# Optimization experiments

Hardware: AMD Instinct MI355X
Metric: run time of the kernel (lower is better)

Reference implementation:

```python
import jax, jax.numpy as jnp
import numpy as np

B, N, F, DM, DMO, OM, L = 32, 64, 64, 128, 64, 128, 4
PRE_H, PRE_O, POST_H = 128, 64, 64
E = N * N
EPS = 1e-5


def swish(x):
    return x * jax.nn.sigmoid(x)


def bn_edges(x, g, b):
    # BatchNorm1d(num_features=E) applied to [B, E, D]: per-edge-channel stats over (batch, D)
    m = x.mean(axis=(0, 2), keepdims=True)
    v = x.var(axis=(0, 2), keepdims=True)
    return (x - m) / jnp.sqrt(v + EPS) * g[None, :, None] + b[None, :, None]


def setup_inputs():
    key = jax.random.key(0)
    ks = iter(jax.random.split(key, 64))

    def rn(shape, s=0.05):
        return jax.random.normal(next(ks), shape, dtype=jnp.float32) * s

    # fully-connected graph incl. self-loops (required by BatchNorm1d(n_nodes^2))
    src, dst = np.meshgrid(np.arange(N), np.arange(N), indexing='ij')
    edge_index = jnp.asarray(np.stack([src.reshape(-1), dst.reshape(-1)]), dtype=jnp.int32)
    return {
        'node_feature': rn((B, N, F), 1.0),
        'vectors': rn((B, N, OM), 1.0),
        'edge_index': edge_index,
        'msg_W1': rn((L, 2 * F, DM)), 'msg_b1': rn((L, DM)),
        'bn1_g': jnp.ones((L, E), jnp.float32), 'bn1_b': jnp.zeros((L, E), jnp.float32),
        'msg_W2': rn((L, DM, DM)), 'msg_b2': rn((L, DM)),
        'bn2_g': jnp.ones((L, E), jnp.float32), 'bn2_b': jnp.zeros((L, E), jnp.float32),
        'msg_W3': rn((L, DM, DM)), 'msg_b3': rn((L, DM)),
        'bn3_g': jnp.ones((L, E), jnp.float32), 'bn3_b': jnp.zeros((L, E), jnp.float32),
        'msg_W4': rn((L, DM, DMO)), 'msg_b4': rn((L, DMO)),
        'upd_W1': rn((L, OM + F + DMO, DM)), 'upd_b1': rn((L, DM)),
        'upd_W2': rn((L, DM, DM)), 'upd_b2': rn((L, DM)),
        'upd_W3': rn((L, DM, DM)), 'upd_b3': rn((L, DM)),
        'upd_W4': rn((L, DM, F)), 'upd_b4': rn((L, F)),
        'pre_W1': rn((F, PRE_H)), 'pre_b1': rn((PRE_H,)),
        'pre_W2': rn((PRE_H, PRE_H)), 'pre_b2': rn((PRE_H,)),
        'pre_W3': rn((PRE_H, PRE_H)), 'pre_b3': rn((PRE_H,)),
        'pre_W4': rn((PRE_H, PRE_O)), 'pre_b4': rn((PRE_O,)),
        'post_W1': rn((PRE_O, POST_H)), 'post_b1': rn((POST_H,)),
        'post_W2': rn((POST_H, 1)), 'post_b2': rn((1,)),
    }


def reference(node_feature, vectors, edge_index,
              msg_W1, msg_b1, bn1_g, bn1_b, msg_W2, msg_b2, bn2_g, bn2_b,
              msg_W3, msg_b3, bn3_g, bn3_b, msg_W4, msg_b4,
              upd_W1, upd_b1, upd_W2, upd_b2, upd_W3, upd_b3, upd_W4, upd_b4,
              pre_W1, pre_b1, pre_W2, pre_b2, pre_W3, pre_b3, pre_W4, pre_b4,
              post_W1, post_b1, post_W2, post_b2):
    src, dst = edge_index[0], edge_index[1]
    x = node_feature  # [B, N, F]
    v = vectors       # [B, N, OM]
    cnt = jax.ops.segment_sum(jnp.ones((E,), jnp.float32), dst, num_segments=N)
    inv_cnt = 1.0 / jnp.maximum(cnt, 1.0)
    for l in range(L):
        x_i = x[:, dst]  # [B, E, F] gather targets
        x_j = x[:, src]  # [B, E, F] gather sources
        h = swish(jnp.concatenate([x_i, x_j], -1) @ msg_W1[l] + msg_b1[l])
        h = bn_edges(h, bn1_g[l], bn1_b[l])
        h = bn_edges(swish(h @ msg_W2[l] + msg_b2[l]), bn2_g[l], bn2_b[l])
        h = bn_edges(swish(h @ msg_W3[l] + msg_b3[l]), bn3_g[l], bn3_b[l])
        m = swish(h @ msg_W4[l] + msg_b4[l])  # [B, E, DMO]
        agg = jax.ops.segment_sum(jnp.transpose(m, (1, 0, 2)), dst, num_segments=N)
        agg = jnp.transpose(agg, (1, 0, 2)) * inv_cnt[None, :, None]  # mean aggr, [B, N, DMO]
        u = jnp.concatenate([v, x, agg], -1)  # [B, N, OM+F+DMO]
        h = swish(u @ upd_W1[l] + upd_b1[l])
        h = swish(h @ upd_W2[l] + upd_b2[l])
        h = swish(h @ upd_W3[l] + upd_b3[l])
        x = x + swish(h @ upd_W4[l] + upd_b4[l])  # residual update
    h = swish(x @ pre_W1 + pre_b1)
    h = swish(h @ pre_W2 + pre_b2)
    h = swish(h @ pre_W3 + pre_b3)
    h = h @ pre_W4 + pre_b4
    c = swish(h @ post_W1 + post_b1) @ post_W2 + post_b2  # [B, N, 1]
    x3 = jnp.einsum('bnd,bn->bd', v, c[..., 0])           # coefficient-weighted vector sum
    return x3, v, c
```

## Files before the change

kernel.cpp:

```cpp
#include <hip/hip_runtime.h>
#include <hip/hip_bf16.h>

typedef unsigned short u16t;
typedef __attribute__((ext_vector_type(8))) short bf16x8;
typedef __attribute__((ext_vector_type(4))) short bf16x4;
typedef __attribute__((ext_vector_type(4))) float f32x4;

#define Bn 32
#define Nn 64
#define Fd 64
#define DMd 128
#define DMOd 64
#define OMd 128
#define En 4096

#define NTEN 36
#define TOTALC 1073217
#define HP 136
#define UP 264
#define XP 72
#define WSEG 131072

__device__ const int kOffs[NTEN + 1] = {
    0,        131072,   393216,   458752,   459264,   475648,   492032,   557568,
    558080,   574464,   590848,   656384,   656896,   673280,   689664,   722432,
    722688,   853760,   854272,   919808,   920320,   985856,   986368,   1019136,
    1019392,  1027584,  1027712,  1044096,  1044224,  1060608,  1060736,  1068928,
    1068992,  1073088,  1073152,  1073216,  1073217
};

#define C_NF    0
#define C_VEC   131072
#define C_MW1   393216
#define C_MB1   458752
#define C_G1    459264
#define C_BB1   475648
#define C_MW2   492032
#define C_MB2   557568
#define C_G2    558080
#define C_BB2   574464
#define C_MW3   590848
#define C_MB3   656384
#define C_G3    656896
#define C_BB3   673280
#define C_MW4   689664
#define C_MB4   722432
#define C_UW1   722688
#define C_UB1   853760
#define C_UW2   854272
#define C_UB2   919808
#define C_UW3   920320
#define C_UB3   985856
#define C_UW4   986368
#define C_UB4   1019136
#define C_PW1   1019392
#define C_PB1   1027584
#define C_PW2   1027712
#define C_PB2   1044096
#define C_PW3   1044224
#define C_PB3   1060608
#define C_PW4   1060736
#define C_PB4   1068928
#define C_QW1   1068992
#define C_QB1   1073088
#define C_QW2   1073152
#define C_QB2   1073216

#define S_W2T 0
#define S_W3T 16384
#define S_W4T 32768
#define S_U1T 40960
#define S_U2T 73728
#define S_U3T 90112
#define S_U4T 106496
#define S_W1T 114688

struct Ptrs { const void* p[NTEN]; };

__device__ __forceinline__ float us2f(u16t u) {
    return __uint_as_float(((unsigned int)u) << 16);
}
__device__ __forceinline__ u16t f2us(float f) {
    __hip_bfloat16 h = __float2bfloat16(f);
    return *reinterpret_cast<u16t*>(&h);
}
__device__ __forceinline__ float swishf(float x) {
    return x * __builtin_amdgcn_rcpf(1.0f + __expf(-x));
}

__global__ void k_flag(const u16t* __restrict__ g1raw, int* __restrict__ flag) {
    if (threadIdx.x == 0) *flag = (g1raw[0] == 0x3F80u) ? 1 : 0;
}

__global__ __launch_bounds__(256) void k_convert(Ptrs t, float* __restrict__ C,
                                                 float* __restrict__ x,
                                                 const int* __restrict__ flagp) {
    int i = blockIdx.x * 256 + threadIdx.x;
    if (i >= TOTALC) return;
    const int flag = *flagp;
    int lo = 0, hi = NTEN;
    while (hi - lo > 1) { int m = (lo + hi) >> 1; if (i >= kOffs[m]) lo = m; else hi = m; }
    const int local = i - kOffs[lo];
    float v;
    if (flag) v = us2f(((const u16t*)t.p[lo])[local]);
    else      v = ((const float*)t.p[lo])[local];
    C[i] = v;
    if (i < Bn * Nn * Fd) x[i] = v;
}

__global__ __launch_bounds__(256) void k_prepw(const float* __restrict__ C,
                                               u16t* __restrict__ W) {
    int i = blockIdx.x * 256 + threadIdx.x;
    if (i >= 4 * WSEG) return;
    const int l = i / WSEG;
    int r = i - l * WSEG;
    int src;
    if (r < S_W3T)      { int q = r;          int n = q >> 7, k = q & 127; src = C_MW2 + l*16384 + k*128 + n; }
    else if (r < S_W4T) { int q = r - S_W3T;  int n = q >> 7, k = q & 127; src = C_MW3 + l*16384 + k*128 + n; }
    else if (r < S_U1T) { int q = r - S_W4T;  int n = q >> 7, k = q & 127; src = C_MW4 + l*8192  + k*64  + n; }
    else if (r < S_U2T) { int q = r - S_U1T;  int n = q >> 8, k = q & 255; src = C_UW1 + l*32768 + k*128 + n; }
    else if (r < S_U3T) { int q = r - S_U2T;  int n = q >> 7, k = q & 127; src = C_UW2 + l*16384 + k*128 + n; }
    else if (r < S_U4T) { int q = r - S_U3T;  int n = q >> 7, k = q & 127; src = C_UW3 + l*16384 + k*128 + n; }
    else if (r < S_W1T) { int q = r - S_U4T;  int n = q >> 7, k = q & 127; src = C_UW4 + l*8192  + k*64  + n; }
    else                { int q = r - S_W1T;  int n = q >> 7, k = q & 127; src = C_MW1 + l*16384 + k*128 + n; }
    W[i] = f2us(C[src]);
}

__global__ __launch_bounds__(256) void k_cs(const u16t* __restrict__ Wt,
                                            float* __restrict__ CS) {
    const int i = blockIdx.x * 256 + threadIdx.x;
    if (i >= 4 * 320) return;
    const int l = i / 320, j = i - l * 320;
    const u16t* base = Wt + l * WSEG +
        (j < 128 ? S_W2T + j * 128
                 : (j < 256 ? S_W3T + (j - 128) * 128
                            : S_W4T + (j - 256) * 128));
    float s = 0.f;
    #pragma unroll 8
    for (int k = 0; k < 128; k++) s += us2f(base[k]);
    CS[i] = s;
}

__global__ __launch_bounds__(128) void k_pq0(const float* __restrict__ x,
                                             const float* __restrict__ W1,
                                             float* __restrict__ P, float* __restrict__ Q,
                                             float* __restrict__ agg) {
    const int gid = blockIdx.x * 128 + threadIdx.x;
    if (gid < Bn * Nn * DMOd) agg[gid] = 0.f;
    __shared__ float xr[Fd];
    const int bn = blockIdx.x;
    const int tid = threadIdx.x;
    if (tid < Fd) xr[tid] = x[bn * Fd + tid];
    __syncthreads();
    float accP = 0.f, accQ = 0.f;
    #pragma unroll
    for (int k = 0; k < Fd; k++) {
        float xv = xr[k];
        accP += xv * W1[k * DMd + tid];
        accQ += xv * W1[(Fd + k) * DMd + tid];
    }
    P[bn * DMd + tid] = accP;
    Q[bn * DMd + tid] = accQ;
}

__device__ __forceinline__ void wave_red8(float* s, float (*rd)[8], int wv, int lane) {
    #pragma unroll
    for (int off = 32; off > 0; off >>= 1)
        #pragma unroll
        for (int k = 0; k < 8; k++) s[k] += __shfl_down(s[k], off);
    if (lane == 0) {
        #pragma unroll
        for (int k = 0; k < 8; k++) rd[wv][k] = s[k];
    }
}

__device__ __forceinline__ void calc_ab(const float (*rd)[8],
                                        const float* __restrict__ g,
                                        const float* __restrict__ bb,
                                        int src0, int dst,
                                        float* a, float* c) {
    #pragma unroll
    for (int e = 0; e < 4; e++) {
        float S  = rd[0][2*e]   + rd[1][2*e]   + rd[2][2*e]   + rd[3][2*e];
        float S2 = rd[0][2*e+1] + rd[1][2*e+1] + rd[2][2*e+1] + rd[3][2*e+1];
        float mean = S * (1.0f / 4096.0f);
        float var  = S2 * (1.0f / 4096.0f) - mean * mean;
        float av = rsqrtf(var + 1e-5f) * g[(src0 + e) * Nn + dst];
        a[e] = av;
        c[e] = bb[(src0 + e) * Nn + dst] - mean * av;
    }
}

__global__ __launch_bounds__(256, 3) void k_edge(
    const float* __restrict__ P, const float* __restrict__ Q,
    const float* __restrict__ b1v,
    const float* __restrict__ g1, const float* __restrict__ bb1,
    const u16t* __restrict__ W2t, const float* __restrict__ b2v, const float* __restrict__ cs2,
    const float* __restrict__ g2, const float* __restrict__ bb2,
    const u16t* __restrict__ W3t, const float* __restrict__ b3v, const float* __restrict__ cs3,
    const float* __restrict__ g3, const float* __restrict__ bb3,
    const u16t* __restrict__ W4t, const float* __restrict__ b4v, const float* __restrict__ cs4,
    float* __restrict__ agg) {
    __shared__ u16t hE[4][Bn * HP];
    __shared__ float red[2][4][8];

    const int dst = blockIdx.x & 63, src0 = (blockIdx.x >> 6) * 4;
    const int tid = threadIdx.x;
    const int wv = tid >> 6, lane = tid & 63, quad = lane >> 4, l15 = lane & 15;
    const int mw = wv & 1, nb2 = wv >> 1;
    const int mrow = mw * 16 + l15;
    const int nBase = nb2 * 64;

    {
        const int b = tid >> 3, d0 = (tid & 7) * 16;
        float4 pv[4], bv4[4];
        {
            const float4* pp = (const float4*)&P[(b * Nn + dst) * DMd + d0];
            const float4* bp = (const float4*)&b1v[d0];
            #pragma unroll
            for (int j = 0; j < 4; j++) { pv[j] = pp[j]; bv4[j] = bp[j]; }
        }
        float s[8];
        #pragma unroll
        for (int e = 0; e < 4; e++) {
            const float4* qq = (const float4*)&Q[(b * Nn + src0 + e) * DMd + d0];
            float u[16];
            #pragma unroll
            for (int j = 0; j < 4; j++) {
                float4 qv = qq[j];
                u[j*4+0] = swishf(pv[j].x + qv.x + bv4[j].x);
                u[j*4+1] = swishf(pv[j].y + qv.y + bv4[j].y);
                u[j*4+2] = swishf(pv[j].z + qv.z + bv4[j].z);
                u[j*4+3] = swishf(pv[j].w + qv.w + bv4[j].w);
            }
            float se = 0.f, s2e = 0.f;
            #pragma unroll
            for (int i = 0; i < 16; i++) { se += u[i]; s2e += u[i] * u[i]; }
            bf16x8 s0, s1;
            #pragma unroll
            for (int j = 0; j < 8; j++) {
                s0[j] = (short)f2us(u[j]);
                s1[j] = (short)f2us(u[8 + j]);
            }
            *(bf16x8*)&hE[e][b * HP + d0]     = s0;
            *(bf16x8*)&hE[e][b * HP + d0 + 8] = s1;
            s[2*e] = se; s[2*e+1] = s2e;
        }
        wave_red8(s, red[0], wv, lane);
    }
    __syncthreads();

    float aP[4], cP[4];
    calc_ab(red[0], g1, bb1, src0, dst, aP, cP);

    #pragma unroll 1
    for (int st = 0; st < 2; st++) {
        const u16t*  Wt = st ? W3t : W2t;
        const float* bv = st ? b3v : b2v;
        const float* cv = st ? cs3 : cs2;
        f32x4 acc[4][4];
        #pragma unroll
        for (int e = 0; e < 4; e++)
            #pragma unroll
            for (int t = 0; t < 4; t++) acc[e][t] = (f32x4){0.f, 0.f, 0.f, 0.f};
        #pragma unroll
        for (int ks = 0; ks < 4; ks++) {
            bf16x8 wb[4];
            #pragma unroll
            for (int t = 0; t < 4; t++)
                wb[t] = *(const bf16x8*)&Wt[(nBase + t * 16 + l15) * 128 + ks * 32 + quad * 8];
            #pragma unroll
            for (int e = 0; e < 4; e++) {
                bf16x8 a8 = *(const bf16x8*)&hE[e][mrow * HP + ks * 32 + quad * 8];
                #pragma unroll
                for (int t = 0; t < 4; t++)
                    acc[e][t] = __builtin_amdgcn_mfma_f32_16x16x32_bf16(wb[t], a8, acc[e][t], 0, 0, 0);
            }
        }
        float4 c4[4], bb4[4];
        #pragma unroll
        for (int t = 0; t < 4; t++) {
            const int n0 = nBase + t * 16 + quad * 4;
            c4[t]  = *(const float4*)&cv[n0];
            bb4[t] = *(const float4*)&bv[n0];
        }
        float s[8];
        #pragma unroll
        for (int e = 0; e < 4; e++) {
            const float ae = aP[e], ce = cP[e];
            float se = 0.f, s2e = 0.f;
            #pragma unroll
            for (int t = 0; t < 4; t++) {
                #pragma unroll
                for (int r = 0; r < 4; r++) {
                    float z = ae * acc[e][t][r] + (ce * (&c4[t].x)[r] + (&bb4[t].x)[r]);
                    float u = swishf(z);
                    acc[e][t][r] = u;
                    se += u; s2e += u * u;
                }
            }
            s[2*e] = se; s[2*e+1] = s2e;
        }
        wave_red8(s, red[1 - st], wv, lane);
        __syncthreads();
        calc_ab(red[1 - st], st ? g3 : g2, st ? bb3 : bb2, src0, dst, aP, cP);
        #pragma unroll
        for (int e = 0; e < 4; e++)
            #pragma unroll
            for (int t = 0; t < 4; t++) {
                bf16x4 pk;
                #pragma unroll
                for (int r = 0; r < 4; r++) pk[r] = (short)f2us(acc[e][t][r]);
                *(bf16x4*)&hE[e][mrow * HP + nBase + t * 16 + quad * 4] = pk;
            }
        __syncthreads();
    }

    {
        const int n40 = nb2 * 32;
        f32x4 a4[4][2];
        #pragma unroll
        for (int e = 0; e < 4; e++) {
            a4[e][0] = (f32x4){0.f, 0.f, 0.f, 0.f};
            a4[e][1] = (f32x4){0.f, 0.f, 0.f, 0.f};
        }
        #pragma unroll
        for (int ks = 0; ks < 4; ks++) {
            bf16x8 wb[2];
            #pragma unroll
            for (int t = 0; t < 2; t++)
                wb[t] = *(const bf16x8*)&W4t[(n40 + t * 16 + l15) * 128 + ks * 32 + quad * 8];
            #pragma unroll
            for (int e = 0; e < 4; e++) {
                bf16x8 a8 = *(const bf16x8*)&hE[e][mrow * HP + ks * 32 + quad * 8];
                #pragma unroll
                for (int t = 0; t < 2; t++)
                    a4[e][t] = __builtin_amdgcn_mfma_f32_16x16x32_bf16(a8, wb[t], a4[e][t], 0, 0, 0);
            }
        }
        #pragma unroll
        for (int t = 0; t < 2; t++) {
            const int col = n40 + t * 16 + l15;
            const float csv = cs4[col], bvv = b4v[col];
            float fe[4];
            #pragma unroll
            for (int e = 0; e < 4; e++) fe[e] = cP[e] * csv + bvv;
            #pragma unroll
            for (int r = 0; r < 4; r++) {
                float m = swishf(aP[0] * a4[0][t][r] + fe[0])
                        + swishf(aP[1] * a4[1][t][r] + fe[1])
                        + swishf(aP[2] * a4[2][t][r] + fe[2])
                        + swishf(aP[3] * a4[3][t][r] + fe[3]);
                const int b = mw * 16 + quad * 4 + r;
                atomicAdd(&agg[(b * Nn + dst) * DMOd + col], m);
            }
        }
    }
}

__global__ __launch_bounds__(256, 4) void k_updq(
    const float* __restrict__ vC, float* __restrict__ x, float* __restrict__ agg,
    const u16t* __restrict__ U1t, const float* __restrict__ b1,
    const u16t* __restrict__ U2t, const float* __restrict__ b2,
    const u16t* __restrict__ U3t, const float* __restrict__ b3,
    const u16t* __restrict__ U4t, const float* __restrict__ b4,
    const u16t* __restrict__ W1Tn, float* __restrict__ Pn, float* __restrict__ Qn,
    int doPQ) {
    __shared__ u16t uL[16 * UP];
    __shared__ u16t hL[16 * HP];
    __shared__ u16t xL[16 * XP];
    const int g0 = blockIdx.x * 16;
    const int tid = threadIdx.x;
    const int wv = tid >> 6, lane = tid & 63, quad = lane >> 4, l15 = lane & 15;
    const int nBase = wv * 32;

    {
        const int i = tid >> 4, c0 = (tid & 15) * 16;
        const int g = g0 + i;
        const float* srcp; float scl = 1.f;
        if (c0 < 128)       srcp = &vC[g * OMd + c0];
        else if (c0 < 192)  srcp = &x[g * Fd + (c0 - 128)];
        else              { srcp = &agg[g * DMOd + (c0 - 192)]; scl = 1.0f / 64.0f; }
        bf16x8 s0, s1;
        #pragma unroll
        for (int j = 0; j < 8; j++) {
            s0[j] = (short)f2us(srcp[j] * scl);
            s1[j] = (short)f2us(srcp[8 + j] * scl);
        }
        *(bf16x8*)&uL[i * UP + c0]     = s0;
        *(bf16x8*)&uL[i * UP + c0 + 8] = s1;
    }
    __syncthreads();

    {
        f32x4 acc[2];
        #pragma unroll
        for (int t = 0; t < 2; t++) {
            float b0 = b1[nBase + t * 16 + l15];
            acc[t] = (f32x4){b0, b0, b0, b0};
        }
        #pragma unroll
        for (int ks = 0; ks < 8; ks++) {
            bf16x8 a8 = *(const bf16x8*)&uL[l15 * UP + ks * 32 + quad * 8];
            #pragma unroll
            for (int t = 0; t < 2; t++) {
                bf16x8 b8 = *(const bf16x8*)&U1t[(nBase + t * 16 + l15) * 256 + ks * 32 + quad * 8];
                acc[t] = __builtin_amdgcn_mfma_f32_16x16x32_bf16(a8, b8, acc[t], 0, 0, 0);
            }
        }
        #pragma unroll
        for (int t = 0; t < 2; t++)
            #pragma unroll
            for (int r = 0; r < 4; r++)
                hL[(quad * 4 + r) * HP + nBase + t * 16 + l15] = f2us(swishf(acc[t][r]));
    }
    __syncthreads();

    #pragma unroll 1
    for (int st = 0; st < 2; st++) {
        const u16t*  Ut = st ? U3t : U2t;
        const float* bb = st ? b3  : b2;
        f32x4 acc[2];
        #pragma unroll
        for (int t = 0; t < 2; t++) {
            float b0 = bb[nBase + t * 16 + l15];
            acc[t] = (f32x4){b0, b0, b0, b0};
        }
        #pragma unroll
        for (int ks = 0; ks < 4; ks++) {
            bf16x8 a8 = *(const bf16x8*)&hL[l15 * HP + ks * 32 + quad * 8];
            #pragma unroll
            for (int t = 0; t < 2; t++) {
                bf16x8 b8 = *(const bf16x8*)&Ut[(nBase + t * 16 + l15) * 128 + ks * 32 + quad * 8];
                acc[t] = __builtin_amdgcn_mfma_f32_16x16x32_bf16(a8, b8, acc[t], 0, 0, 0);
            }
        }
        __syncthreads();
        #pragma unroll
        for (int t = 0; t < 2; t++)
            #pragma unroll
            for (int r = 0; r < 4; r++)
                hL[(quad * 4 + r) * HP + nBase + t * 16 + l15] = f2us(swishf(acc[t][r]));
        __syncthreads();
    }

    {
        const int n4 = wv * 16;
        f32x4 acc;
        {
            float b0 = b4[n4 + l15];
            acc = (f32x4){b0, b0, b0, b0};
        }
        #pragma unroll
        for (int ks = 0; ks < 4; ks++) {
            bf16x8 a8 = *(const bf16x8*)&hL[l15 * HP + ks * 32 + quad * 8];
            bf16x8 b8 = *(const bf16x8*)&U4t[(n4 + l15) * 128 + ks * 32 + quad * 8];
            acc = __builtin_amdgcn_mfma_f32_16x16x32_bf16(a8, b8, acc, 0, 0, 0);
        }
        #pragma unroll
        for (int r = 0; r < 4; r++) {
            int row = quad * 4 + r, col = n4 + l15;
            float xn = x[(g0 + row) * Fd + col] + swishf(acc[r]);
            x[(g0 + row) * Fd + col] = xn;
            xL[row * XP + col] = f2us(xn);
        }
    }

    {
        int idx = tid;
        #pragma unroll
        for (int k = 0; k < 4; k++, idx += 256) agg[g0 * DMOd + idx] = 0.f;
    }
    __syncthreads();

    if (doPQ) {
        f32x4 ap[2], aq[2];
        #pragma unroll
        for (int j = 0; j < 2; j++) { ap[j] = (f32x4){0,0,0,0}; aq[j] = (f32x4){0,0,0,0}; }
        #pragma unroll
        for (int ks = 0; ks < 2; ks++) {
            bf16x8 a8 = *(const bf16x8*)&xL[l15 * XP + ks * 32 + quad * 8];
            #pragma unroll
            for (int j = 0; j < 2; j++) {
                const int n0 = (wv * 2 + j) * 16 + l15;
                bf16x8 bp = *(const bf16x8*)&W1Tn[n0 * 128 + ks * 32 + quad * 8];
                bf16x8 bq = *(const bf16x8*)&W1Tn[n0 * 128 + 64 + ks * 32 + quad * 8];
                ap[j] = __builtin_amdgcn_mfma_f32_16x16x32_bf16(a8, bp, ap[j], 0, 0, 0);
                aq[j] = __builtin_amdgcn_mfma_f32_16x16x32_bf16(a8, bq, aq[j], 0, 0, 0);
            }
        }
        #pragma unroll
        for (int j = 0; j < 2; j++)
            #pragma unroll
            for (int r = 0; r < 4; r++) {
                int g = g0 + quad * 4 + r, col = (wv * 2 + j) * 16 + l15;
                Pn[g * DMd + col] = ap[j][r];
                Qn[g * DMd + col] = aq[j][r];
            }
    }
}

__global__ __launch_bounds__(128) void k_final(
    const float* __restrict__ x, const void* __restrict__ vraw,
    const float* __restrict__ pW1, const float* __restrict__ pb1,
    const float* __restrict__ pW2, const float* __restrict__ pb2,
    const float* __restrict__ pW3, const float* __restrict__ pb3,
    const float* __restrict__ pW4, const float* __restrict__ pb4,
    const float* __restrict__ qW1, const float* __restrict__ qb1,
    const float* __restrict__ qW2, const float* __restrict__ qb2,
    float* __restrict__ c_buf, void* __restrict__ out, const int* __restrict__ flagp) {
    __shared__ float xr[64];
    __shared__ float ha[128];
    __shared__ float hb[128];
    __shared__ float hc[64];
    __shared__ float tt[64];
    const int bn = blockIdx.x;
    const int tid = threadIdx.x;
    const int flag = *flagp;
    if (tid < 64) xr[tid] = x[bn * Fd + tid];
    __syncthreads();
    float acc = pb1[tid];
    #pragma unroll 8
    for (int k = 0; k < 64; k++) acc += xr[k] * pW1[k * 128 + tid];
    ha[tid] = swishf(acc);
    __syncthreads();
    acc = pb2[tid];
    #pragma unroll 8
    for (int k = 0; k < 128; k++) acc += ha[k] * pW2[k * 128 + tid];
    hb[tid] = swishf(acc);
    __syncthreads();
    acc = pb3[tid];
    #pragma unroll 8
    for (int k = 0; k < 128; k++) acc += hb[k] * pW3[k * 128 + tid];
    ha[tid] = swishf(acc);
    __syncthreads();
    if (tid < 64) {
        acc = pb4[tid];
        #pragma unroll 8
        for (int k = 0; k < 128; k++) acc += ha[k] * pW4[k * 64 + tid];
        hc[tid] = acc;
    }
    __syncthreads();
    if (tid < 64) {
        acc = qb1[tid];
        #pragma unroll 8
        for (int k = 0; k < 64; k++) acc += hc[k] * qW1[k * 64 + tid];
        tt[tid] = swishf(acc);
    }
    __syncthreads();
    if (tid < 64) {
        float p = tt[tid] * qW2[tid];
        #pragma unroll
        for (int off = 32; off > 0; off >>= 1) p += __shfl_down(p, off);
        if (tid == 0) {
            float cv = p + qb2[0];
            c_buf[bn] = cv;
            const int ci = 4096 + Bn * Nn * OMd + bn;
            if (flag) ((u16t*)out)[ci] = f2us(cv);
            else      ((float*)out)[ci] = cv;
        }
    }
    const int vi = bn * OMd + tid;
    if (flag) ((u16t*)out)[4096 + vi] = ((const u16t*)vraw)[vi];
    else      ((float*)out)[4096 + vi] = ((const float*)vraw)[vi];
}

__global__ __launch_bounds__(128) void k_x3(const float* __restrict__ vC,
                                            const float* __restrict__ c_buf,
                                            void* __restrict__ out,
                                            const int* __restrict__ flagp) {
    const int b = blockIdx.x, d = threadIdx.x;
    const int flag = *flagp;
    float acc = 0.f;
    #pragma unroll 4
    for (int n = 0; n < Nn; n++)
        acc += vC[(b * Nn + n) * OMd + d] * c_buf[b * Nn + n];
    if (flag) ((u16t*)out)[b * OMd + d] = f2us(acc);
    else      ((float*)out)[b * OMd + d] = acc;
}

extern "C" void kernel_launch(void* const* d_in, const int* in_sizes, int n_in,
                              void* d_out, int out_size, void* d_ws, size_t ws_size,
                              hipStream_t stream) {
    float* ws = (float*)d_ws;
    int*   flag  = (int*)d_ws;
    float* C     = ws + 16;
    float* x     = C + 1073664;
    float* P     = x + 131072;
    float* Q     = P + 262144;
    float* agg   = Q + 262144;
    float* c_buf = agg + 131072;
    u16t*  Wt    = (u16t*)(c_buf + 2048);
    float* CS    = (float*)(Wt + 4 * WSEG);

    Ptrs t;
    for (int i = 0, j = 0; i < 37; i++) {
        if (i == 2) continue;
        t.p[j++] = d_in[i];
    }

    k_flag<<<1, 64, 0, stream>>>((const u16t*)d_in[5], flag);
    k_convert<<<(TOTALC + 255) / 256, 256, 0, stream>>>(t, C, x, flag);
    k_prepw<<<(4 * WSEG + 255) / 256, 256, 0, stream>>>(C, Wt);
    k_cs<<<5, 256, 0, stream>>>(Wt, CS);
    k_pq0<<<Bn * Nn, 128, 0, stream>>>(x, C + C_MW1, P, Q, agg);

    for (int l = 0; l < 4; l++) {
        u16t* Wl = Wt + l * WSEG;
        float* CSl = CS + l * 320;
        k_edge<<<64 * 16, 256, 0, stream>>>(
            P, Q,
            C + C_MB1 + l * DMd, C + C_G1 + l * En, C + C_BB1 + l * En,
            Wl + S_W2T, C + C_MB2 + l * DMd, CSl,
            C + C_G2 + l * En, C + C_BB2 + l * En,
            Wl + S_W3T, C + C_MB3 + l * DMd, CSl + 128,
            C + C_G3 + l * En, C + C_BB3 + l * En,
            Wl + S_W4T, C + C_MB4 + l * DMOd, CSl + 256,
            agg);
        const int doPQ = (l < 3) ? 1 : 0;
        const u16t* W1Tn = Wt + (doPQ ? (l + 1) : 0) * WSEG + S_W1T;
        k_updq<<<Bn * Nn / 16, 256, 0, stream>>>(
            C + C_VEC, x, agg,
            Wl + S_U1T, C + C_UB1 + l * DMd,
            Wl + S_U2T, C + C_UB2 + l * DMd,
            Wl + S_U3T, C + C_UB3 + l * DMd,
            Wl + S_U4T, C + C_UB4 + l * DMOd,
            W1Tn, P, Q, doPQ);
    }

    k_final<<<Bn * Nn, 128, 0, stream>>>(x, d_in[1],
        C + C_PW1, C + C_PB1, C + C_PW2, C + C_PB2,
        C + C_PW3, C + C_PB3, C + C_PW4, C + C_PB4,
        C + C_QW1, C + C_QB1, C + C_QW2, C + C_QB2,
        c_buf, d_out, flag);
    k_x3<<<Bn, 128, 0, stream>>>(C + C_VEC, c_buf, d_out, flag);
}
```

Baseline: 377.6 us.

## Merge preprocessing kernels into one launch and cut k_edge register pressure

Five setup kernels (flag, convert, weight transpose, column sums, P/Q init) become one k_prep launch whose branches each read the raw inputs directly, so they no longer depend on earlier converted buffers. The flag is recomputed inline from the raw tensor rather than read from a workspace value. k_edge's MFMA accumulation is split into two halves of edges, with results packed into bf16 registers, and its launch-bounds occupancy hint is raised from 3 to 4. This removes launch gaps and dependencies between the prep stages and aims for more resident waves in k_edge, at the risk of register spills and extra reloads of the bias and column-sum vectors.

```diff
diff --git a/kernel.cpp b/kernel.cpp
--- a/kernel.cpp
+++ b/kernel.cpp
@@ -75,6 +75,12 @@
 #define S_U4T 106496
 #define S_W1T 114688
 
+#define NB_CONV 4193
+#define NB_PREPW 2048
+#define NB_CS 5
+#define NB_PQ0 1024
+#define NB_PREP (NB_CONV + NB_PREPW + NB_CS + NB_PQ0)
+
 struct Ptrs { const void* p[NTEN]; };
 
 __device__ __forceinline__ float us2f(u16t u) {
@@ -87,80 +93,89 @@
 __device__ __forceinline__ float swishf(float x) {
     return x * __builtin_amdgcn_rcpf(1.0f + __expf(-x));
 }
-
-__global__ void k_flag(const u16t* __restrict__ g1raw, int* __restrict__ flag) {
-    if (threadIdx.x == 0) *flag = (g1raw[0] == 0x3F80u) ? 1 : 0;
-}
-
-__global__ __launch_bounds__(256) void k_convert(Ptrs t, float* __restrict__ C,
-                                                 float* __restrict__ x,
-                                                 const int* __restrict__ flagp) {
-    int i = blockIdx.x * 256 + threadIdx.x;
-    if (i >= TOTALC) return;
-    const int flag = *flagp;
-    int lo = 0, hi = NTEN;
-    while (hi - lo > 1) { int m = (lo + hi) >> 1; if (i >= kOffs[m]) lo = m; else hi = m; }
-    const int local = i - kOffs[lo];
-    float v;
-    if (flag) v = us2f(((const u16t*)t.p[lo])[local]);
-    else      v = ((const float*)t.p[lo])[local];
-    C[i] = v;
-    if (i < Bn * Nn * Fd) x[i] = v;
-}
-
-__global__ __launch_bounds__(256) void k_prepw(const float* __restrict__ C,
-                                               u16t* __restrict__ W) {
-    int i = blockIdx.x * 256 + threadIdx.x;
-    if (i >= 4 * WSEG) return;
-    const int l = i / WSEG;
-    int r = i - l * WSEG;
-    int src;
-    if (r < S_W3T)      { int q = r;          int n = q >> 7, k = q & 127; src = C_MW2 + l*16384 + k*128 + n; }
-    else if (r < S_W4T) { int q = r - S_W3T;  int n = q >> 7, k = q & 127; src = C_MW3 + l*16384 + k*128 + n; }
-    else if (r < S_U1T) { int q = r - S_W4T;  int n = q >> 7, k = q & 127; src = C_MW4 + l*8192  + k*64  + n; }
-    else if (r < S_U2T) { int q = r - S_U1T;  int n = q >> 8, k = q & 255; src = C_UW1 + l*32768 + k*128 + n; }
-    else if (r < S_U3T) { int q = r - S_U2T;  int n = q >> 7, k = q & 127; src = C_UW2 + l*16384 + k*128 + n; }
-    else if (r < S_U4T) { int q = r - S_U3T;  int n = q >> 7, k = q & 127; src = C_UW3 + l*16384 + k*128 + n; }
-    else if (r < S_W1T) { int q = r - S_U4T;  int n = q >> 7, k = q & 127; src = C_UW4 + l*8192  + k*64  + n; }
-    else                { int q = r - S_W1T;  int n = q >> 7, k = q & 127; src = C_MW1 + l*16384 + k*128 + n; }
-    W[i] = f2us(C[src]);
-}
-
-__global__ __launch_bounds__(256) void k_cs(const u16t* __restrict__ Wt,
-                                            float* __restrict__ CS) {
-    const int i = blockIdx.x * 256 + threadIdx.x;
-    if (i >= 4 * 320) return;
-    const int l = i / 320, j = i - l * 320;
-    const u16t* base = Wt + l * WSEG +
-        (j < 128 ? S_W2T + j * 128
-                 : (j < 256 ? S_W3T + (j - 128) * 128
-                            : S_W4T + (j - 256) * 128));
-    float s = 0.f;
-    #pragma unroll 8
-    for (int k = 0; k < 128; k++) s += us2f(base[k]);
-    CS[i] = s;
-}
-
-__global__ __launch_bounds__(128) void k_pq0(const float* __restrict__ x,
-                                             const float* __restrict__ W1,
-                                             float* __restrict__ P, float* __restrict__ Q,
-                                             float* __restrict__ agg) {
-    const int gid = blockIdx.x * 128 + threadIdx.x;
-    if (gid < Bn * Nn * DMOd) agg[gid] = 0.f;
-    __shared__ float xr[Fd];
-    const int bn = blockIdx.x;
+__device__ __forceinline__ float ldcvt(const void* p, int idx, int flag) {
+    return flag ? us2f(((const u16t*)p)[idx]) : ((const float*)p)[idx];
+}
+__device__ __forceinline__ int get_flag(const void* g1raw) {
+    return (((const u16t*)g1raw)[0] == 0x3F80u) ? 1 : 0;
+}
+
+__global__ __launch_bounds__(256) void k_prep(Ptrs t, float* __restrict__ C,
+                                              float* __restrict__ x,
+                                              u16t* __restrict__ W,
+                                              float* __restrict__ CS,
+                                              float* __restrict__ P,
+                                              float* __restrict__ Q,
+                                              float* __restrict__ agg) {
+    const int flag = get_flag(t.p[4]);
+    const int blk = blockIdx.x;
     const int tid = threadIdx.x;
-    if (tid < Fd) xr[tid] = x[bn * Fd + tid];
-    __syncthreads();
-    float accP = 0.f, accQ = 0.f;
-    #pragma unroll
-    for (int k = 0; k < Fd; k++) {
-        float xv = xr[k];
-        accP += xv * W1[k * DMd + tid];
-        accQ += xv * W1[(Fd + k) * DMd + tid];
-    }
-    P[bn * DMd + tid] = accP;
-    Q[bn * DMd + tid] = accQ;
+
+    if (blk < NB_CONV) {
+        int i = blk * 256 + tid;
+        if (i >= TOTALC) return;
+        int lo = 0, hi = NTEN;
+        while (hi - lo > 1) { int m = (lo + hi) >> 1; if (i >= kOffs[m]) lo = m; else hi = m; }
+        const int local = i - kOffs[lo];
+        float v = ldcvt(t.p[lo], local, flag);
+        C[i] = v;
+        if (i < Bn * Nn * Fd) x[i] = v;
+    } else if (blk < NB_CONV + NB_PREPW) {
+        int i = (blk - NB_CONV) * 256 + tid;
+        const int l = i / WSEG;
+        int r = i - l * WSEG;
+        int tens, local;
+        if (r < S_W3T)      { int q = r;          int n = q >> 7, k = q & 127; tens = 6;  local = l*16384 + k*128 + n; }
+        else if (r < S_W4T) { int q = r - S_W3T;  int n = q >> 7, k = q & 127; tens = 10; local = l*16384 + k*128 + n; }
+        else if (r < S_U1T) { int q = r - S_W4T;  int n = q >> 7, k = q & 127; tens = 14; local = l*8192  + k*64  + n; }
+        else if (r < S_U2T) { int q = r - S_U1T;  int n = q >> 8, k = q & 255; tens = 16; local = l*32768 + k*128 + n; }
+        else if (r < S_U3T) { int q = r - S_U2T;  int n = q >> 7, k = q & 127; tens = 18; local = l*16384 + k*128 + n; }
+        else if (r < S_U4T) { int q = r - S_U3T;  int n = q >> 7, k = q & 127; tens = 20; local = l*16384 + k*128 + n; }
+        else if (r < S_W1T) { int q = r - S_U4T;  int n = q >> 7, k = q & 127; tens = 22; local = l*8192  + k*64  + n; }
+        else                { int q = r - S_W1T;  int n = q >> 7, k = q & 127; tens = 2;  local = l*16384 + k*128 + n; }
+        W[i] = f2us(ldcvt(t.p[tens], local, flag));
+    } else if (blk < NB_CONV + NB_PREPW + NB_CS) {
+        int i = (blk - NB_CONV - NB_PREPW) * 256 + tid;
+        if (i >= 4 * 320) return;
+        const int l = i / 320, j = i - l * 320;
+        const void* tp; int base, stride;
+        if (j < 128)      { tp = t.p[6];  base = l*16384 + j;         stride = 128; }
+        else if (j < 256) { tp = t.p[10]; base = l*16384 + (j - 128); stride = 128; }
+        else              { tp = t.p[14]; base = l*8192  + (j - 256); stride = 64; }
+        float s = 0.f;
+        #pragma unroll 8
+        for (int k = 0; k < 128; k++) s += us2f(f2us(ldcvt(tp, base + k * stride, flag)));
+        CS[i] = s;
+    } else {
+        const int rel = blk - (NB_CONV + NB_PREPW + NB_CS);
+        const int gid = rel * 256 + tid;
+        if (gid < Bn * Nn * DMOd) agg[gid] = 0.f;
+        __shared__ float xr2[2][Fd];
+        const int half = tid >> 7, t7 = tid & 127;
+        const int bn = rel * 2 + half;
+        if (t7 < Fd) xr2[half][t7] = ldcvt(t.p[0], bn * Fd + t7, flag);
+        __syncthreads();
+        float accP = 0.f, accQ = 0.f;
+        if (flag) {
+            const u16t* W1 = (const u16t*)t.p[2];
+            #pragma unroll 8
+            for (int k = 0; k < Fd; k++) {
+                float xv = xr2[half][k];
+                accP += xv * us2f(W1[k * DMd + t7]);
+                accQ += xv * us2f(W1[(Fd + k) * DMd + t7]);
+            }
+        } else {
+            const float* W1 = (const float*)t.p[2];
+            #pragma unroll 8
+            for (int k = 0; k < Fd; k++) {
+                float xv = xr2[half][k];
+                accP += xv * W1[k * DMd + t7];
+                accQ += xv * W1[(Fd + k) * DMd + t7];
+            }
+        }
+        P[bn * DMd + t7] = accP;
+        Q[bn * DMd + t7] = accQ;
+    }
 }
 
 __device__ __forceinline__ void wave_red8(float* s, float (*rd)[8], int wv, int lane) {
@@ -191,7 +206,7 @@
     }
 }
 
-__global__ __launch_bounds__(256, 3) void k_edge(
+__global__ __launch_bounds__(256, 4) void k_edge(
     const float* __restrict__ P, const float* __restrict__ Q,
     const float* __restrict__ b1v,
     const float* __restrict__ g1, const float* __restrict__ bb1,
@@ -258,48 +273,49 @@
         const u16t*  Wt = st ? W3t : W2t;
         const float* bv = st ? b3v : b2v;
         const float* cv = st ? cs3 : cs2;
-        f32x4 acc[4][4];
-        #pragma unroll
-        for (int e = 0; e < 4; e++)
-            #pragma unroll
-            for (int t = 0; t < 4; t++) acc[e][t] = (f32x4){0.f, 0.f, 0.f, 0.f};
-        #pragma unroll
-        for (int ks = 0; ks < 4; ks++) {
-            bf16x8 wb[4];
-            #pragma unroll
-            for (int t = 0; t < 4; t++)
-                wb[t] = *(const bf16x8*)&Wt[(nBase + t * 16 + l15) * 128 + ks * 32 + quad * 8];
-            #pragma unroll
-            for (int e = 0; e < 4; e++) {
-                bf16x8 a8 = *(const bf16x8*)&hE[e][mrow * HP + ks * 32 + quad * 8];
+        bf16x4 pk[4][4];
+        float s[8];
+        #pragma unroll
+        for (int eh = 0; eh < 2; eh++) {
+            f32x4 acc[2][4];
+            #pragma unroll
+            for (int ee = 0; ee < 2; ee++)
+                #pragma unroll
+                for (int t = 0; t < 4; t++) acc[ee][t] = (f32x4){0.f, 0.f, 0.f, 0.f};
+            #pragma unroll
+            for (int ks = 0; ks < 4; ks++) {
+                bf16x8 wb[4];
                 #pragma unroll
                 for (int t = 0; t < 4; t++)
-                    acc[e][t] = __builtin_amdgcn_mfma_f32_16x16x32_bf16(wb[t], a8, acc[e][t], 0, 0, 0);
-            }
-        }
-        float4 c4[4], bb4[4];
-        #pragma unroll
-        for (int t = 0; t < 4; t++) {
-            const int n0 = nBase + t * 16 + quad * 4;
-            c4[t]  = *(const float4*)&cv[n0];
-            bb4[t] = *(const float4*)&bv[n0];
-        }
-        float s[8];
-        #pragma unroll
-        for (int e = 0; e < 4; e++) {
-            const float ae = aP[e], ce = cP[e];
-            float se = 0.f, s2e = 0.f;
-            #pragma unroll
-            for (int t = 0; t < 4; t++) {
+                    wb[t] = *(const bf16x8*)&Wt[(nBase + t * 16 + l15) * 128 + ks * 32 + quad * 8];
                 #pragma unroll
-                for (int r = 0; r < 4; r++) {
-                    float z = ae * acc[e][t][r] + (ce * (&c4[t].x)[r] + (&bb4[t].x)[r]);
-                    float u = swishf(z);
-                    acc[e][t][r] = u;
-                    se += u; s2e += u * u;
+                for (int ee = 0; ee < 2; ee++) {
+                    bf16x8 a8 = *(const bf16x8*)&hE[eh * 2 + ee][mrow * HP + ks * 32 + quad * 8];
+                    #pragma unroll
+                    for (int t = 0; t < 4; t++)
+                        acc[ee][t] = __builtin_amdgcn_mfma_f32_16x16x32_bf16(wb[t], a8, acc[ee][t], 0, 0, 0);
                 }
             }
-            s[2*e] = se; s[2*e+1] = s2e;
+            #pragma unroll
+            for (int ee = 0; ee < 2; ee++) {
+                const int e = eh * 2 + ee;
+                const float ae = aP[e], ce = cP[e];
+                float se = 0.f, s2e = 0.f;
+                #pragma unroll
+                for (int t = 0; t < 4; t++) {
+                    const int n0 = nBase + t * 16 + quad * 4;
+                    float4 c4  = *(const float4*)&cv[n0];
+                    float4 bb4 = *(const float4*)&bv[n0];
+                    #pragma unroll
+                    for (int r = 0; r < 4; r++) {
+                        float z = ae * acc[ee][t][r] + (ce * (&c4.x)[r] + (&bb4.x)[r]);
+                        float u = swishf(z);
+                        se += u; s2e += u * u;
+                        pk[e][t][r] = (short)f2us(u);
+                    }
+                }
+                s[2*e] = se; s[2*e+1] = s2e;
+            }
         }
         wave_red8(s, red[1 - st], wv, lane);
         __syncthreads();
@@ -307,12 +323,8 @@
         #pragma unroll
         for (int e = 0; e < 4; e++)
             #pragma unroll
-            for (int t = 0; t < 4; t++) {
-                bf16x4 pk;
-                #pragma unroll
-                for (int r = 0; r < 4; r++) pk[r] = (short)f2us(acc[e][t][r]);
-                *(bf16x4*)&hE[e][mrow * HP + nBase + t * 16 + quad * 4] = pk;
-            }
+            for (int t = 0; t < 4; t++)
+                *(bf16x4*)&hE[e][mrow * HP + nBase + t * 16 + quad * 4] = pk[e][t];
         __syncthreads();
     }
 
@@ -508,7 +520,7 @@
     const float* __restrict__ pW4, const float* __restrict__ pb4,
     const float* __restrict__ qW1, const float* __restrict__ qb1,
     const float* __restrict__ qW2, const float* __restrict__ qb2,
-    float* __restrict__ c_buf, void* __restrict__ out, const int* __restrict__ flagp) {
+    float* __restrict__ c_buf, void* __restrict__ out, const void* __restrict__ g1raw) {
     __shared__ float xr[64];
     __shared__ float ha[128];
     __shared__ float hb[128];
@@ -516,7 +528,7 @@
     __shared__ float tt[64];
     const int bn = blockIdx.x;
     const int tid = threadIdx.x;
-    const int flag = *flagp;
+    const int flag = get_flag(g1raw);
     if (tid < 64) xr[tid] = x[bn * Fd + tid];
     __syncthreads();
     float acc = pb1[tid];
@@ -568,9 +580,9 @@
 __global__ __launch_bounds__(128) void k_x3(const float* __restrict__ vC,
                                             const float* __restrict__ c_buf,
                                             void* __restrict__ out,
-                                            const int* __restrict__ flagp) {
+                                            const void* __restrict__ g1raw) {
     const int b = blockIdx.x, d = threadIdx.x;
-    const int flag = *flagp;
+    const int flag = get_flag(g1raw);
     float acc = 0.f;
     #pragma unroll 4
     for (int n = 0; n < Nn; n++)
@@ -583,7 +595,6 @@
                               void* d_out, int out_size, void* d_ws, size_t ws_size,
                               hipStream_t stream) {
     float* ws = (float*)d_ws;
-    int*   flag  = (int*)d_ws;
     float* C     = ws + 16;
     float* x     = C + 1073664;
     float* P     = x + 131072;
@@ -599,11 +610,7 @@
         t.p[j++] = d_in[i];
     }
 
-    k_flag<<<1, 64, 0, stream>>>((const u16t*)d_in[5], flag);
-    k_convert<<<(TOTALC + 255) / 256, 256, 0, stream>>>(t, C, x, flag);
-    k_prepw<<<(4 * WSEG + 255) / 256, 256, 0, stream>>>(C, Wt);
-    k_cs<<<5, 256, 0, stream>>>(Wt, CS);
-    k_pq0<<<Bn * Nn, 128, 0, stream>>>(x, C + C_MW1, P, Q, agg);
+    k_prep<<<NB_PREP, 256, 0, stream>>>(t, C, x, Wt, CS, P, Q, agg);
 
     for (int l = 0; l < 4; l++) {
         u16t* Wl = Wt + l * WSEG;
@@ -632,6 +639,6 @@
         C + C_PW1, C + C_PB1, C + C_PW2, C + C_PB2,
         C + C_PW3, C + C_PB3, C + C_PW4, C + C_PB4,
         C + C_QW1, C + C_QB1, C + C_QW2, C + C_QB2,
-        c_buf, d_out, flag);
-    k_x3<<<Bn, 128, 0, stream>>>(C + C_VEC, c_buf, d_out, flag);
-}
+        c_buf, d_out, d_in[5]);
+    k_x3<<<Bn, 128, 0, stream>>>(C + C_VEC, c_buf, d_out, d_in[5]);
+}
```

Measured after the change: 386.3 us. 1.02x slower.
